# Performance work log

Hardware: AMD Instinct MI355X
Metric: run time of the kernel (lower is better)

Reference implementation:

```python
import jax, jax.numpy as jnp
import numpy as np

N = 100000   # nodes
E = 1600000  # edges
F = 128      # input features
H = 128      # hidden
L = 4        # num_layers (1 conv1 + 3 convs)
S = 10000    # subgraphs
G = 256      # graphs
C = 10       # classes
BN_EPS = 1e-5


def setup_inputs() -> dict:
    key = jax.random.key(0)
    ks = jax.random.split(key, 12)
    x = jax.random.normal(ks[0], (N, F), jnp.float32)
    edge_index = jax.random.randint(ks[1], (2, E), 0, N, jnp.int32)
    node_to_subgraph = jnp.sort(jax.random.randint(ks[2], (N,), 0, S, jnp.int32))
    subgraph_to_graph = jnp.sort(jax.random.randint(ks[3], (S,), 0, G, jnp.int32))
    sc = 1.0 / np.sqrt(H)
    # stacked per-layer GIN MLP params (torch Linear layout [out, in]); F == H so conv1 stacks too
    W1 = jax.random.uniform(ks[4], (L, H, F), jnp.float32, -sc, sc)
    b1 = jax.random.uniform(ks[5], (L, H), jnp.float32, -sc, sc)
    g1 = jnp.ones((L, H), jnp.float32)
    be1 = jnp.zeros((L, H), jnp.float32)
    W2 = jax.random.uniform(ks[6], (L, H, H), jnp.float32, -sc, sc)
    b2 = jax.random.uniform(ks[7], (L, H), jnp.float32, -sc, sc)
    g2 = jnp.ones((L, H), jnp.float32)
    be2 = jnp.zeros((L, H), jnp.float32)
    eps = jnp.zeros((L,), jnp.float32)  # train_eps=True, init 0
    sc1 = 1.0 / np.sqrt(L * H)
    lin1_W = jax.random.uniform(ks[8], (H, L * H), jnp.float32, -sc1, sc1)
    lin1_b = jax.random.uniform(ks[9], (H,), jnp.float32, -sc1, sc1)
    lin2_W = jax.random.uniform(ks[10], (C, H), jnp.float32, -sc, sc)
    lin2_b = jax.random.uniform(ks[11], (C,), jnp.float32, -sc, sc)
    return dict(x=x, edge_index=edge_index, node_to_subgraph=node_to_subgraph,
                subgraph_to_graph=subgraph_to_graph, W1=W1, b1=b1, g1=g1, be1=be1,
                W2=W2, b2=b2, g2=g2, be2=be2, eps=eps,
                lin1_W=lin1_W, lin1_b=lin1_b, lin2_W=lin2_W, lin2_b=lin2_b)


def _bn(h, g, b):
    mu = h.mean(axis=0)
    var = jnp.mean((h - mu) ** 2, axis=0)  # biased var (training-mode BN)
    return (h - mu) * jax.lax.rsqrt(var + BN_EPS) * g + b


def _seg_mean(f, seg, num_segments):
    s = jax.ops.segment_sum(f, seg, num_segments=num_segments)
    cnt = jax.ops.segment_sum(jnp.ones((f.shape[0], 1), f.dtype), seg, num_segments=num_segments)
    return s / jnp.maximum(cnt, 1.0)


def reference(x, edge_index, node_to_subgraph, subgraph_to_graph,
              W1, b1, g1, be1, W2, b2, g2, be2, eps,
              lin1_W, lin1_b, lin2_W, lin2_b):
    src, dst = edge_index[0], edge_index[1]

    def layer(xc, p):
        w1, bb1, gg1, bt1, w2, bb2, gg2, bt2, e = p
        agg = jax.ops.segment_sum(xc[src], dst, num_segments=N)  # neighbor sum
        h = (1.0 + e) * xc + agg
        h = jax.nn.relu(_bn(h @ w1.T + bb1, gg1, bt1))
        h = jax.nn.relu(_bn(h @ w2.T + bb2, gg2, bt2))
        return h, h

    _, ys = jax.lax.scan(layer, x, (W1, b1, g1, be1, W2, b2, g2, be2, eps))  # [L, N, H]
    feat = jnp.transpose(ys, (1, 0, 2)).reshape(N, L * H)  # torch.cat(xs, dim=1)
    sub = _seg_mean(feat, node_to_subgraph, S)   # [S, L*H]
    gph = _seg_mean(sub, subgraph_to_graph, G)   # [G, L*H]
    h = jax.nn.relu(gph @ lin1_W.T + lin1_b)
    out = h @ lin2_W.T + lin2_b                  # dropout inactive in eval
    return jax.nn.log_softmax(out, axis=-1)
```

## Files before the change

### kernel.cpp

```cpp
#include <hip/hip_runtime.h>

typedef unsigned int u32;
typedef unsigned short u16;

#define NN 100000
#define EE 1600000
#define SS 10000
#define GG 256
#define NSCAN ((NN + 1023) / 1024)
#define NCHUNK 16

#define O_W1   0
#define O_B1   65536
#define O_G1   66048
#define O_BE1  66560
#define O_W2   67072
#define O_B2   132608
#define O_G2   133120
#define O_BE2  133632
#define O_EPS  134144
#define O_L1W  134148
#define O_L1B  199684
#define O_L2W  199812
#define O_L2B  201092
#define NPAR   201102

typedef __bf16 bf16x8_t __attribute__((ext_vector_type(8)));
typedef float f32x4_t __attribute__((ext_vector_type(4)));
typedef u32 u32x4_t __attribute__((ext_vector_type(4)));

__device__ __forceinline__ float bf2f(u16 u) {
  union { u32 i; float f; } x; x.i = ((u32)u) << 16; return x.f;
}
__device__ __forceinline__ u16 f2bf(float f) {
  union { float f; u32 i; } x; x.f = f;
  u32 r = x.i + 0x7fffu + ((x.i >> 16) & 1u);
  return (u16)(r >> 16);
}
__device__ __forceinline__ int lbound(const int* __restrict__ a, int n, int key) {
  int lo = 0, hi = n;
  while (lo < hi) { int mid = (lo + hi) >> 1; if (a[mid] < key) lo = mid + 1; else hi = mid; }
  return lo;
}

__global__ void k_sniff(const u16* __restrict__ x, int* __restrict__ flag) {
  __shared__ int cnt;
  if (threadIdx.x == 0) cnt = 0;
  __syncthreads();
  int weird = 0;
  for (int i = threadIdx.x; i < 8192; i += 256) {
    u16 v = x[i];
    int e = (v >> 7) & 0xff;
    if (e >= 0xC0) weird++;
  }
  atomicAdd(&cnt, weird);
  __syncthreads();
  if (threadIdx.x == 0) *flag = (cnt > 64) ? 1 : 0;
}

__global__ __launch_bounds__(256) void k_cvt_params(
    const void* pW1, const void* pb1, const void* pg1, const void* pbe1,
    const void* pW2, const void* pb2, const void* pg2, const void* pbe2,
    const void* peps, const void* pl1w, const void* pl1b, const void* pl2w, const void* pl2b,
    const int* __restrict__ flagp, float* __restrict__ P) {
  int i = blockIdx.x * 256 + threadIdx.x;
  if (i >= NPAR) return;
  const void* src; int rel;
  if      (i < O_B1)  { src = pW1;  rel = i - O_W1; }
  else if (i < O_G1)  { src = pb1;  rel = i - O_B1; }
  else if (i < O_BE1) { src = pg1;  rel = i - O_G1; }
  else if (i < O_W2)  { src = pbe1; rel = i - O_BE1; }
  else if (i < O_B2)  { src = pW2;  rel = i - O_W2; }
  else if (i < O_G2)  { src = pb2;  rel = i - O_B2; }
  else if (i < O_BE2) { src = pg2;  rel = i - O_G2; }
  else if (i < O_EPS) { src = pbe2; rel = i - O_BE2; }
  else if (i < O_L1W) { src = peps; rel = i - O_EPS; }
  else if (i < O_L1B) { src = pl1w; rel = i - O_L1W; }
  else if (i < O_L2W) { src = pl1b; rel = i - O_L1B; }
  else if (i < O_L2B) { src = pl2w; rel = i - O_L2W; }
  else                { src = pl2b; rel = i - O_L2B; }
  float v = (*flagp) ? ((const float*)src)[rel] : bf2f(((const u16*)src)[rel]);
  P[i] = v;
}

__global__ __launch_bounds__(256) void k_cvtW(const float* __restrict__ P,
                                              u16* __restrict__ W1b, u16* __restrict__ W2b) {
  int i = blockIdx.x * 256 + threadIdx.x;
  if (i >= 131072) return;
  if (i < 65536) W1b[i] = f2bf(P[O_W1 + i]);
  else           W2b[i - 65536] = f2bf(P[O_W2 + i - 65536]);
}

__global__ __launch_bounds__(256) void k_prep(const void* __restrict__ x, const int* __restrict__ flagp,
                                              u16* __restrict__ Z0) {
  int i = blockIdx.x * 256 + threadIdx.x;
  if (i >= (NN * 128) / 8) return;
  if (*flagp) {
    const float4* xf = (const float4*)x;
    float4 a = xf[i * 2], b = xf[i * 2 + 1];
    u32x4_t o;
    o[0] = (u32)f2bf(a.x) | ((u32)f2bf(a.y) << 16);
    o[1] = (u32)f2bf(a.z) | ((u32)f2bf(a.w) << 16);
    o[2] = (u32)f2bf(b.x) | ((u32)f2bf(b.y) << 16);
    o[3] = (u32)f2bf(b.z) | ((u32)f2bf(b.w) << 16);
    *(u32x4_t*)(Z0 + i * 8) = o;
  } else {
    *(u32x4_t*)(Z0 + i * 8) = ((const u32x4_t*)x)[i];
  }
}

__global__ __launch_bounds__(256) void k_hist12(const int* __restrict__ src, const int* __restrict__ dst,
                                                int* __restrict__ cnt, int* __restrict__ cnt2) {
  int i = blockIdx.x * 256 + threadIdx.x;
  if (i >= EE) return;
  int d = dst[i], s = src[i];
  atomicAdd(&cnt[d], 1);
  atomicAdd(&cnt2[d * NCHUNK + (s >> 13)], 1);
}

__global__ __launch_bounds__(256) void k_scan1(const int* __restrict__ cnt, int* __restrict__ bsum) {
  __shared__ int sh[256];
  int base = blockIdx.x * 1024 + threadIdx.x * 4;
  int s = 0;
#pragma unroll
  for (int i = 0; i < 4; i++) { int idx = base + i; s += (idx < NN) ? cnt[idx] : 0; }
  sh[threadIdx.x] = s; __syncthreads();
  for (int o = 128; o > 0; o >>= 1) {
    if (threadIdx.x < o) sh[threadIdx.x] += sh[threadIdx.x + o];
    __syncthreads();
  }
  if (threadIdx.x == 0) bsum[blockIdx.x] = sh[0];
}

__global__ void k_scan2(int* __restrict__ bsum, int* __restrict__ off) {
  if (threadIdx.x == 0 && blockIdx.x == 0) {
    int run = 0;
    for (int i = 0; i < NSCAN; i++) { int v = bsum[i]; bsum[i] = run; run += v; }
    off[NN] = run;
  }
}

__global__ __launch_bounds__(256) void k_scan3(const int* __restrict__ cnt, const int* __restrict__ bsum,
                                               int* __restrict__ off) {
  __shared__ int sh[256];
  int base = blockIdx.x * 1024 + threadIdx.x * 4;
  int v[4]; int s = 0;
#pragma unroll
  for (int i = 0; i < 4; i++) { int idx = base + i; v[i] = (idx < NN) ? cnt[idx] : 0; s += v[i]; }
  sh[threadIdx.x] = s; __syncthreads();
  for (int o = 1; o < 256; o <<= 1) {
    int add = (threadIdx.x >= o) ? sh[threadIdx.x - o] : 0;
    __syncthreads();
    sh[threadIdx.x] += add;
    __syncthreads();
  }
  int run = sh[threadIdx.x] - s + bsum[blockIdx.x];
#pragma unroll
  for (int i = 0; i < 4; i++) { int idx = base + i; if (idx < NN) { off[idx] = run; run += v[i]; } }
}

__global__ __launch_bounds__(256) void k_start2(const int* __restrict__ off, const int* __restrict__ cnt2,
                                                int* __restrict__ start2) {
  int d = blockIdx.x * 256 + threadIdx.x;
  if (d >= NN) return;
  int base = off[d];
#pragma unroll
  for (int c = 0; c < NCHUNK; c++) {
    int s = cnt2[d * NCHUNK + c];
    start2[d * NCHUNK + c] = base;
    base += s;
  }
}

__global__ __launch_bounds__(256) void k_fill2(const int* __restrict__ src, const int* __restrict__ dst,
                                               int* __restrict__ start2, int* __restrict__ csr) {
  int i = blockIdx.x * 256 + threadIdx.x;
  if (i >= EE) return;
  int d = dst[i], s = src[i];
  int p = atomicAdd(&start2[d * NCHUNK + (s >> 13)], 1);
  csr[p] = s;
}

__global__ __launch_bounds__(256) void k_agg_gemm(
    const u16* __restrict__ Z, const int* __restrict__ off, const int* __restrict__ csr,
    const u16* __restrict__ Wb, const float* __restrict__ bias, const float* __restrict__ P,
    int layer, int mode, const float* __restrict__ st_prev, const float* __restrict__ gw,
    const float* __restrict__ bw, u16* __restrict__ H, float* __restrict__ st) {
  __shared__ __align__(16) u16 lds[4][16][136];
  __shared__ __align__(16) int shidx[4][512];
  int wave = threadIdx.x >> 6, lane = threadIdx.x & 63;
  int r0 = blockIdx.x * 64 + wave * 16;
  float ev = 1.0f + P[O_EPS + layer];
  const u32* zr = (const u32*)Z;

  int c0 = 2 * lane, c1 = 2 * lane + 1;
  float scl0 = 1.f, scl1 = 1.f, sh0 = 0.f, sh1 = 0.f, ncl = -3.0e38f;
  if (mode) {
    float mu0 = st_prev[c0] * (1.0f / NN);
    float v0 = fmaxf(st_prev[128 + c0] * (1.0f / NN) - mu0 * mu0, 0.f);
    scl0 = gw[c0] * rsqrtf(v0 + 1e-5f);
    sh0 = bw[c0] - mu0 * scl0;
    float mu1 = st_prev[c1] * (1.0f / NN);
    float v1 = fmaxf(st_prev[128 + c1] * (1.0f / NN) - mu1 * mu1, 0.f);
    scl1 = gw[c1] * rsqrtf(v1 + 1e-5f);
    sh1 = bw[c1] - mu1 * scl1;
    ncl = 0.f;
  }

  int offv = 0;
  if (lane <= 16) {
    int rr = r0 + lane; if (rr > NN) rr = NN; if (rr < 0) rr = 0;
    offv = off[rr];
  }
  int ebase = __shfl(offv, 0, 64);
  int eend  = __shfl(offv, 16, 64);
  int tn = eend - ebase;
  int nst = tn < 512 ? tn : 512;
  for (int i = lane; i < nst; i += 64) shidx[wave][i] = csr[ebase + i];

  for (int rr = 0; rr < 16; rr++) {
    int row = r0 + rr;
    float a0 = 0.f, a1 = 0.f;
    if (row < NN) {
      int s = __shfl(offv, rr, 64), e = __shfl(offv, rr + 1, 64);
      int n = e - s, b = s - ebase;
      u32 d = zr[row * 64 + lane];
      a0 = ev * fmaxf(fmaf(bf2f((u16)(d & 0xffffu)), scl0, sh0), ncl);
      a1 = ev * fmaxf(fmaf(bf2f((u16)(d >> 16)), scl1, sh1), ncl);
      const int* ip = (b + n <= 512) ? &shidx[wave][b] : &csr[s];
      int i = 0;
      for (; i + 7 < n; i += 8) {
        u32 dd[8];
#pragma unroll
        for (int j = 0; j < 8; j++) dd[j] = zr[ip[i + j] * 64 + lane];
#pragma unroll
        for (int j = 0; j < 8; j++) {
          a0 += fmaxf(fmaf(bf2f((u16)(dd[j] & 0xffffu)), scl0, sh0), ncl);
          a1 += fmaxf(fmaf(bf2f((u16)(dd[j] >> 16)), scl1, sh1), ncl);
        }
      }
      for (; i + 1 < n; i += 2) {
        u32 d0 = zr[ip[i] * 64 + lane];
        u32 d1 = zr[ip[i + 1] * 64 + lane];
        a0 += fmaxf(fmaf(bf2f((u16)(d0 & 0xffffu)), scl0, sh0), ncl) +
              fmaxf(fmaf(bf2f((u16)(d1 & 0xffffu)), scl1 * 0.f + scl0, sh0), ncl);
        a1 += fmaxf(fmaf(bf2f((u16)(d0 >> 16)), scl1, sh1), ncl) +
              fmaxf(fmaf(bf2f((u16)(d1 >> 16)), scl1, sh1), ncl);
      }
      if (i < n) {
        u32 d0 = zr[ip[i] * 64 + lane];
        a0 += fmaxf(fmaf(bf2f((u16)(d0 & 0xffffu)), scl0, sh0), ncl);
        a1 += fmaxf(fmaf(bf2f((u16)(d0 >> 16)), scl1, sh1), ncl);
      }
    }
    ((u32*)&lds[wave][rr][0])[lane] = (u32)f2bf(a0) | ((u32)f2bf(a1) << 16);
  }

  int nidx = lane & 15, q = lane >> 4;
  f32x4_t acc[8];
  f32x4_t z4 = {0.f, 0.f, 0.f, 0.f};
#pragma unroll
  for (int ot = 0; ot < 8; ot++) acc[ot] = z4;
#pragma unroll
  for (int ks = 0; ks < 4; ks++) {
    bf16x8_t af = __builtin_bit_cast(bf16x8_t, *(const u32x4_t*)&lds[wave][nidx][ks * 32 + q * 8]);
#pragma unroll
    for (int ot = 0; ot < 8; ot++) {
      bf16x8_t bfr = __builtin_bit_cast(bf16x8_t, *(const u32x4_t*)(Wb + (ot * 16 + nidx) * 128 + ks * 32 + q * 8));
      acc[ot] = __builtin_amdgcn_mfma_f32_16x16x32_bf16(af, bfr, acc[ot], 0, 0, 0);
    }
  }
  float* sstw = (float*)&shidx[wave][0];
#pragma unroll
  for (int ot = 0; ot < 8; ot++) {
    int col = ot * 16 + nidx;
    float bv = bias[col];
    float s = 0.f, sq = 0.f;
#pragma unroll
    for (int j = 0; j < 4; j++) {
      int row = r0 + q * 4 + j;
      if (row < NN) {
        float v = acc[ot][j] + bv;
        u16 h = f2bf(v);
        float vr = bf2f(h);
        H[row * 128 + col] = h;
        s += vr; sq += vr * vr;
      }
    }
    s  += __shfl_xor(s, 16, 64);  s  += __shfl_xor(s, 32, 64);
    sq += __shfl_xor(sq, 16, 64); sq += __shfl_xor(sq, 32, 64);
    if (q == 0) { sstw[col] = s; sstw[128 + col] = sq; }
  }
  __syncthreads();
  int t = threadIdx.x;
  float tot = ((float*)&shidx[0][0])[t] + ((float*)&shidx[1][0])[t] +
              ((float*)&shidx[2][0])[t] + ((float*)&shidx[3][0])[t];
  atomicAdd(&st[t], tot);
}

__global__ __launch_bounds__(256) void k_bn_gemm(
    const u16* __restrict__ Hin, const u16* __restrict__ Wb, const float* __restrict__ bias,
    const float* __restrict__ st_in, const float* __restrict__ gw, const float* __restrict__ bw,
    u16* __restrict__ Hout, float* __restrict__ st_out) {
  __shared__ float sc[256];
  __shared__ float sst[4][256];
  int t = threadIdx.x;
  if (t < 128) {
    float mu = st_in[t] * (1.0f / NN);
    float var = st_in[128 + t] * (1.0f / NN) - mu * mu;
    var = fmaxf(var, 0.f);
    float r = rsqrtf(var + 1e-5f);
    float scl = gw[t] * r;
    sc[t] = scl;
    sc[128 + t] = bw[t] - mu * scl;
  }
  __syncthreads();
  int wave = t >> 6, lane = t & 63;
  int r0 = blockIdx.x * 64 + wave * 16;
  int nidx = lane & 15, q = lane >> 4;
  int arow = r0 + nidx;
  u32x4_t zero4 = {0, 0, 0, 0};
  u32x4_t raw[4];
#pragma unroll
  for (int ks = 0; ks < 4; ks++)
    raw[ks] = (arow < NN) ? *(const u32x4_t*)(Hin + arow * 128 + ks * 32 + q * 8) : zero4;
  f32x4_t acc[8];
  f32x4_t z4 = {0.f, 0.f, 0.f, 0.f};
#pragma unroll
  for (int ot = 0; ot < 8; ot++) acc[ot] = z4;
#pragma unroll
  for (int ks = 0; ks < 4; ks++) {
    int k0 = ks * 32 + q * 8;
    u32x4_t ap;
#pragma unroll
    for (int w = 0; w < 4; w++) {
      int k = k0 + 2 * w;
      float v0 = fmaxf(bf2f((u16)(raw[ks][w] & 0xffffu)) * sc[k] + sc[128 + k], 0.f);
      float v1 = fmaxf(bf2f((u16)(raw[ks][w] >> 16)) * sc[k + 1] + sc[128 + k + 1], 0.f);
      ap[w] = (u32)f2bf(v0) | ((u32)f2bf(v1) << 16);
    }
    bf16x8_t af = __builtin_bit_cast(bf16x8_t, ap);
#pragma unroll
    for (int ot = 0; ot < 8; ot++) {
      bf16x8_t bfr = __builtin_bit_cast(bf16x8_t, *(const u32x4_t*)(Wb + (ot * 16 + nidx) * 128 + k0));
      acc[ot] = __builtin_amdgcn_mfma_f32_16x16x32_bf16(af, bfr, acc[ot], 0, 0, 0);
    }
  }
#pragma unroll
  for (int ot = 0; ot < 8; ot++) {
    int col = ot * 16 + nidx;
    float bv = bias[col];
    float s = 0.f, sq = 0.f;
#pragma unroll
    for (int j = 0; j < 4; j++) {
      int row = r0 + q * 4 + j;
      if (row < NN) {
        float v = acc[ot][j] + bv;
        u16 h = f2bf(v);
        float vr = bf2f(h);
        Hout[row * 128 + col] = h;
        s += vr; sq += vr * vr;
      }
    }
    s  += __shfl_xor(s, 16, 64);  s  += __shfl_xor(s, 32, 64);
    sq += __shfl_xor(sq, 16, 64); sq += __shfl_xor(sq, 32, 64);
    if (q == 0) { sst[wave][col] = s; sst[wave][128 + col] = sq; }
  }
  __syncthreads();
  float tot = sst[0][t] + sst[1][t] + sst[2][t] + sst[3][t];
  atomicAdd(&st_out[t], tot);
}

__global__ __launch_bounds__(256) void k_sub(
    const u16* __restrict__ Hin, const float* __restrict__ st_in, const float* __restrict__ gw,
    const float* __restrict__ bw, const int* __restrict__ n2s,
    float* __restrict__ sub, int layer) {
  __shared__ float sc[256];
  int t = threadIdx.x;
  if (t < 128) {
    float mu = st_in[t] * (1.0f / NN);
    float var = st_in[128 + t] * (1.0f / NN) - mu * mu;
    var = fmaxf(var, 0.f);
    float r = rsqrtf(var + 1e-5f);
    float scl = gw[t] * r;
    sc[t] = scl;
    sc[128 + t] = bw[t] - mu * scl;
  }
  __syncthreads();
  int s = (blockIdx.x * 256 + t) >> 6;
  int lane = t & 63;
  if (s >= SS) return;
  int r0 = lbound(n2s, NN, s), r1 = lbound(n2s, NN, s + 1);
  float scl0 = sc[2 * lane], scl1 = sc[2 * lane + 1];
  float sh0 = sc[128 + 2 * lane], sh1 = sc[128 + 2 * lane + 1];
  const u32* hr = (const u32*)Hin;
  float a0 = 0.f, a1 = 0.f;
  for (int r = r0; r < r1; r++) {
    u32 d = hr[r * 64 + lane];
    a0 += fmaxf(bf2f((u16)(d & 0xffffu)) * scl0 + sh0, 0.f);
    a1 += fmaxf(bf2f((u16)(d >> 16)) * scl1 + sh1, 0.f);
  }
  int c = r1 - r0;
  float inv = 1.0f / (float)(c > 0 ? c : 1);
  float2 v; v.x = a0 * inv; v.y = a1 * inv;
  *(float2*)(sub + (size_t)s * 512 + layer * 128 + lane * 2) = v;
}

__global__ __launch_bounds__(256) void k_graphpool(const float* __restrict__ sub, const int* __restrict__ s2g,
                                                   float* __restrict__ gph) {
  int g = (blockIdx.x * 256 + threadIdx.x) >> 6;
  int lane = threadIdx.x & 63;
  if (g >= GG) return;
  int r0 = lbound(s2g, SS, g), r1 = lbound(s2g, SS, g + 1);
  float a[8] = {0.f, 0.f, 0.f, 0.f, 0.f, 0.f, 0.f, 0.f};
  for (int s = r0; s < r1; s++) {
    const float* row = sub + (size_t)s * 512 + lane * 8;
#pragma unroll
    for (int j = 0; j < 8; j++) a[j] += row[j];
  }
  int c = r1 - r0;
  float inv = 1.0f / (float)(c > 0 ? c : 1);
  float* orow = gph + (size_t)g * 512 + lane * 8;
#pragma unroll
  for (int j = 0; j < 8; j++) orow[j] = a[j] * inv;
}

__global__ __launch_bounds__(128) void k_head(const float* __restrict__ gph, const float* __restrict__ P,
                                              const int* __restrict__ flagp, void* __restrict__ out) {
  __shared__ float gsh[512];
  __shared__ float hsh[128];
  __shared__ float lsh[12];
  int g = blockIdx.x, t = threadIdx.x;
  for (int i = t; i < 512; i += 128) gsh[i] = gph[(size_t)g * 512 + i];
  __syncthreads();
  float acc = P[O_L1B + t];
  const float4* wr = (const float4*)(P + O_L1W + t * 512);
  for (int kb = 0; kb < 128; kb++) {
    float4 w = wr[kb];
    int k = kb * 4;
    acc += gsh[k] * w.x + gsh[k + 1] * w.y + gsh[k + 2] * w.z + gsh[k + 3] * w.w;
  }
  hsh[t] = fmaxf(acc, 0.f);
  __syncthreads();
  if (t < 10) {
    float a = P[O_L2B + t];
    const float* w2r = P + O_L2W + t * 128;
    for (int k = 0; k < 128; k++) a += hsh[k] * w2r[k];
    lsh[t] = a;
  }
  __syncthreads();
  if (t == 0) {
    float m = -1e30f;
    for (int c = 0; c < 10; c++) m = fmaxf(m, lsh[c]);
    float se = 0.f;
    for (int c = 0; c < 10; c++) se += expf(lsh[c] - m);
    lsh[10] = m + logf(se);
  }
  __syncthreads();
  if (t < 10) {
    float v = lsh[t] - lsh[10];
    if (*flagp) ((float*)out)[g * 10 + t] = v;
    else        ((u16*)out)[g * 10 + t] = f2bf(v);
  }
}

extern "C" void kernel_launch(void* const* d_in, const int* in_sizes, int n_in,
                              void* d_out, int out_size, void* d_ws, size_t ws_size,
                              hipStream_t stream) {
  const void* x   = d_in[0];
  const int* ei   = (const int*)d_in[1];
  const int* n2s  = (const int*)d_in[2];
  const int* s2g  = (const int*)d_in[3];

  char* ws = (char*)d_ws;
  size_t o = 0;
  auto alloc = [&](size_t b) -> void* {
    void* p = ws + o;
    o += (b + 255) & ~(size_t)255;
    return p;
  };
  int* flag    = (int*)alloc(256);
  int* off     = (int*)alloc((NN + 1) * 4);
  int* cnt     = (int*)alloc(NN * 4);
  int* bsum    = (int*)alloc(NSCAN * 4);
  int* cnt2    = (int*)alloc((size_t)NN * NCHUNK * 4);
  int* start2  = (int*)alloc((size_t)NN * NCHUNK * 4);
  int* csr     = (int*)alloc((size_t)EE * 4);
  u16* Z0      = (u16*)alloc((size_t)NN * 128 * 2);
  u16* H1      = (u16*)alloc((size_t)NN * 128 * 2);
  u16* H2A     = (u16*)alloc((size_t)NN * 128 * 2);
  u16* H2B     = (u16*)alloc((size_t)NN * 128 * 2);
  float* sub   = (float*)alloc((size_t)SS * 512 * 4);
  float* gph   = (float*)alloc((size_t)GG * 512 * 4);
  float* stats = (float*)alloc(8 * 256 * 4);
  float* P     = (float*)alloc((size_t)NPAR * 4);
  u16* W1b     = (u16*)alloc(65536 * 2);
  u16* W2b     = (u16*)alloc(65536 * 2);

  const int* esrc = ei;
  const int* edst = ei + EE;

  hipMemsetAsync(cnt, 0, NN * 4, stream);
  hipMemsetAsync(cnt2, 0, (size_t)NN * NCHUNK * 4, stream);
  hipMemsetAsync(stats, 0, 8 * 256 * 4, stream);

  k_sniff<<<dim3(1), dim3(256), 0, stream>>>((const u16*)x, flag);
  k_cvt_params<<<dim3((NPAR + 255) / 256), dim3(256), 0, stream>>>(
      d_in[4], d_in[5], d_in[6], d_in[7], d_in[8], d_in[9], d_in[10], d_in[11],
      d_in[12], d_in[13], d_in[14], d_in[15], d_in[16], flag, P);
  k_cvtW<<<dim3(512), dim3(256), 0, stream>>>(P, W1b, W2b);
  k_prep<<<dim3((NN * 128 / 8 + 255) / 256), dim3(256), 0, stream>>>(x, flag, Z0);

  k_hist12<<<dim3((EE + 255) / 256), dim3(256), 0, stream>>>(esrc, edst, cnt, cnt2);
  k_scan1<<<dim3(NSCAN), dim3(256), 0, stream>>>(cnt, bsum);
  k_scan2<<<dim3(1), dim3(64), 0, stream>>>(bsum, off);
  k_scan3<<<dim3(NSCAN), dim3(256), 0, stream>>>(cnt, bsum, off);
  k_start2<<<dim3((NN + 255) / 256), dim3(256), 0, stream>>>(off, cnt2, start2);
  k_fill2<<<dim3((EE + 255) / 256), dim3(256), 0, stream>>>(esrc, edst, start2, csr);

  const u16* H2prev = Z0;
  for (int l = 0; l < 4; l++) {
    u16* H2cur = (l & 1) ? H2B : H2A;
    float* st1 = stats + (2 * l) * 256;
    float* st2 = stats + (2 * l + 1) * 256;
    const float* stp = (l > 0) ? (stats + (2 * l - 1) * 256) : P;
    k_agg_gemm<<<dim3((NN + 63) / 64), dim3(256), 0, stream>>>(
        H2prev, off, csr, W1b + l * 16384, P + O_B1 + l * 128, P, l,
        (l > 0) ? 1 : 0, stp, P + O_G2 + (l - 1 >= 0 ? l - 1 : 0) * 128,
        P + O_BE2 + (l - 1 >= 0 ? l - 1 : 0) * 128, H1, st1);
    k_bn_gemm<<<dim3((NN + 63) / 64), dim3(256), 0, stream>>>(
        H1, W2b + l * 16384, P + O_B2 + l * 128, st1, P + O_G1 + l * 128, P + O_BE1 + l * 128, H2cur, st2);
    k_sub<<<dim3((SS + 3) / 4), dim3(256), 0, stream>>>(
        H2cur, st2, P + O_G2 + l * 128, P + O_BE2 + l * 128, n2s, sub, l);
    H2prev = H2cur;
  }
  k_graphpool<<<dim3((GG + 3) / 4), dim3(256), 0, stream>>>(sub, s2g, gph);
  k_head<<<dim3(GG), dim3(128), 0, stream>>>(gph, P, flag, (void*)d_out);
}
```

Baseline: 1.318 ms.

## Gather neighbor rows as 16-byte vectors across four lane slots and simplify CSR build

The aggregation loop now has each lane load 8 bf16 features (16 bytes) per neighbor, with four 16-lane slots handling different neighbors in parallel, then reduces across slots with shuffles. The self term is folded in as neighbor index zero, and the mode flag becomes a template parameter so layer 0 skips the BN/ReLU math. The CSR build drops the per-source-chunk bucketing (cnt2/start2) in favor of a plain atomic fill, which removes a kernel and a large memset but loses the source-sorted neighbor order that may have helped gather locality.

```diff
diff --git a/kernel.cpp b/kernel.cpp
--- a/kernel.cpp
+++ b/kernel.cpp
@@ -8,7 +8,6 @@
 #define SS 10000
 #define GG 256
 #define NSCAN ((NN + 1023) / 1024)
-#define NCHUNK 16
 
 #define O_W1   0
 #define O_B1   65536
@@ -109,13 +108,9 @@
   }
 }
 
-__global__ __launch_bounds__(256) void k_hist12(const int* __restrict__ src, const int* __restrict__ dst,
-                                                int* __restrict__ cnt, int* __restrict__ cnt2) {
+__global__ __launch_bounds__(256) void k_hist(const int* __restrict__ dst, int* __restrict__ cnt) {
   int i = blockIdx.x * 256 + threadIdx.x;
-  if (i >= EE) return;
-  int d = dst[i], s = src[i];
-  atomicAdd(&cnt[d], 1);
-  atomicAdd(&cnt2[d * NCHUNK + (s >> 13)], 1);
+  if (i < EE) atomicAdd(&cnt[dst[i]], 1);
 }
 
 __global__ __launch_bounds__(256) void k_scan1(const int* __restrict__ cnt, int* __restrict__ bsum) {
@@ -159,52 +154,40 @@
   for (int i = 0; i < 4; i++) { int idx = base + i; if (idx < NN) { off[idx] = run; run += v[i]; } }
 }
 
-__global__ __launch_bounds__(256) void k_start2(const int* __restrict__ off, const int* __restrict__ cnt2,
-                                                int* __restrict__ start2) {
-  int d = blockIdx.x * 256 + threadIdx.x;
-  if (d >= NN) return;
-  int base = off[d];
-#pragma unroll
-  for (int c = 0; c < NCHUNK; c++) {
-    int s = cnt2[d * NCHUNK + c];
-    start2[d * NCHUNK + c] = base;
-    base += s;
-  }
-}
-
-__global__ __launch_bounds__(256) void k_fill2(const int* __restrict__ src, const int* __restrict__ dst,
-                                               int* __restrict__ start2, int* __restrict__ csr) {
+__global__ __launch_bounds__(256) void k_fill(const int* __restrict__ src, const int* __restrict__ dst,
+                                              const int* __restrict__ off, int* __restrict__ cur,
+                                              int* __restrict__ csr) {
   int i = blockIdx.x * 256 + threadIdx.x;
   if (i >= EE) return;
-  int d = dst[i], s = src[i];
-  int p = atomicAdd(&start2[d * NCHUNK + (s >> 13)], 1);
-  csr[p] = s;
-}
-
+  int d = dst[i];
+  int p = off[d] + atomicAdd(&cur[d], 1);
+  csr[p] = src[i];
+}
+
+template <int MODE>
 __global__ __launch_bounds__(256) void k_agg_gemm(
     const u16* __restrict__ Z, const int* __restrict__ off, const int* __restrict__ csr,
     const u16* __restrict__ Wb, const float* __restrict__ bias, const float* __restrict__ P,
-    int layer, int mode, const float* __restrict__ st_prev, const float* __restrict__ gw,
+    int layer, const float* __restrict__ st_prev, const float* __restrict__ gw,
     const float* __restrict__ bw, u16* __restrict__ H, float* __restrict__ st) {
   __shared__ __align__(16) u16 lds[4][16][136];
   __shared__ __align__(16) int shidx[4][512];
   int wave = threadIdx.x >> 6, lane = threadIdx.x & 63;
   int r0 = blockIdx.x * 64 + wave * 16;
   float ev = 1.0f + P[O_EPS + layer];
-  const u32* zr = (const u32*)Z;
-
-  int c0 = 2 * lane, c1 = 2 * lane + 1;
-  float scl0 = 1.f, scl1 = 1.f, sh0 = 0.f, sh1 = 0.f, ncl = -3.0e38f;
-  if (mode) {
-    float mu0 = st_prev[c0] * (1.0f / NN);
-    float v0 = fmaxf(st_prev[128 + c0] * (1.0f / NN) - mu0 * mu0, 0.f);
-    scl0 = gw[c0] * rsqrtf(v0 + 1e-5f);
-    sh0 = bw[c0] - mu0 * scl0;
-    float mu1 = st_prev[c1] * (1.0f / NN);
-    float v1 = fmaxf(st_prev[128 + c1] * (1.0f / NN) - mu1 * mu1, 0.f);
-    scl1 = gw[c1] * rsqrtf(v1 + 1e-5f);
-    sh1 = bw[c1] - mu1 * scl1;
-    ncl = 0.f;
+  int slot = lane >> 4;
+  int cb = (lane & 15) * 8;
+
+  float scl[8], shf[8];
+  if (MODE) {
+#pragma unroll
+    for (int k = 0; k < 8; k++) {
+      int c = cb + k;
+      float mu = st_prev[c] * (1.0f / NN);
+      float var = fmaxf(st_prev[128 + c] * (1.0f / NN) - mu * mu, 0.f);
+      float s = gw[c] * rsqrtf(var + 1e-5f);
+      scl[k] = s; shf[k] = bw[c] - mu * s;
+    }
   }
 
   int offv = 0;
@@ -220,40 +203,62 @@
 
   for (int rr = 0; rr < 16; rr++) {
     int row = r0 + rr;
-    float a0 = 0.f, a1 = 0.f;
+    float acc[8];
+#pragma unroll
+    for (int k = 0; k < 8; k++) acc[k] = 0.f;
     if (row < NN) {
       int s = __shfl(offv, rr, 64), e = __shfl(offv, rr + 1, 64);
       int n = e - s, b = s - ebase;
-      u32 d = zr[row * 64 + lane];
-      a0 = ev * fmaxf(fmaf(bf2f((u16)(d & 0xffffu)), scl0, sh0), ncl);
-      a1 = ev * fmaxf(fmaf(bf2f((u16)(d >> 16)), scl1, sh1), ncl);
-      const int* ip = (b + n <= 512) ? &shidx[wave][b] : &csr[s];
-      int i = 0;
-      for (; i + 7 < n; i += 8) {
-        u32 dd[8];
-#pragma unroll
-        for (int j = 0; j < 8; j++) dd[j] = zr[ip[i + j] * 64 + lane];
-#pragma unroll
-        for (int j = 0; j < 8; j++) {
-          a0 += fmaxf(fmaf(bf2f((u16)(dd[j] & 0xffffu)), scl0, sh0), ncl);
-          a1 += fmaxf(fmaf(bf2f((u16)(dd[j] >> 16)), scl1, sh1), ncl);
+      int m = n + 1;
+      auto nbr = [&](int j) -> int {
+        int t = b + j - 1;
+        return (t < 512) ? shidx[wave][t] : csr[ebase + t];
+      };
+      auto consume = [&](u32x4_t d, float c) {
+#pragma unroll
+        for (int k = 0; k < 4; k++) {
+          float v0 = bf2f((u16)(d[k] & 0xffffu));
+          float v1 = bf2f((u16)(d[k] >> 16));
+          if (MODE) {
+            v0 = fmaxf(fmaf(v0, scl[2 * k], shf[2 * k]), 0.f);
+            v1 = fmaxf(fmaf(v1, scl[2 * k + 1], shf[2 * k + 1]), 0.f);
+          }
+          acc[2 * k]     = fmaf(v0, c, acc[2 * k]);
+          acc[2 * k + 1] = fmaf(v1, c, acc[2 * k + 1]);
         }
+      };
+      int g = 0;
+      for (; g + 16 <= m; g += 16) {
+        int j0 = g + slot;
+        int i0 = (j0 == 0) ? row : nbr(j0);
+        int i1 = nbr(j0 + 4), i2 = nbr(j0 + 8), i3 = nbr(j0 + 12);
+        u32x4_t d0 = *(const u32x4_t*)(Z + (size_t)i0 * 128 + cb);
+        u32x4_t d1 = *(const u32x4_t*)(Z + (size_t)i1 * 128 + cb);
+        u32x4_t d2 = *(const u32x4_t*)(Z + (size_t)i2 * 128 + cb);
+        u32x4_t d3 = *(const u32x4_t*)(Z + (size_t)i3 * 128 + cb);
+        consume(d0, (j0 == 0) ? ev : 1.f);
+        consume(d1, 1.f); consume(d2, 1.f); consume(d3, 1.f);
       }
-      for (; i + 1 < n; i += 2) {
-        u32 d0 = zr[ip[i] * 64 + lane];
-        u32 d1 = zr[ip[i + 1] * 64 + lane];
-        a0 += fmaxf(fmaf(bf2f((u16)(d0 & 0xffffu)), scl0, sh0), ncl) +
-              fmaxf(fmaf(bf2f((u16)(d1 & 0xffffu)), scl1 * 0.f + scl0, sh0), ncl);
-        a1 += fmaxf(fmaf(bf2f((u16)(d0 >> 16)), scl1, sh1), ncl) +
-              fmaxf(fmaf(bf2f((u16)(d1 >> 16)), scl1, sh1), ncl);
+      for (; g < m; g += 4) {
+        int j = g + slot;
+        int idx = row; float c = 0.f;
+        if (j < m) { c = 1.f; if (j > 0) idx = nbr(j); else c = ev; }
+        u32x4_t d = *(const u32x4_t*)(Z + (size_t)idx * 128 + cb);
+        consume(d, c);
       }
-      if (i < n) {
-        u32 d0 = zr[ip[i] * 64 + lane];
-        a0 += fmaxf(fmaf(bf2f((u16)(d0 & 0xffffu)), scl0, sh0), ncl);
-        a1 += fmaxf(fmaf(bf2f((u16)(d0 >> 16)), scl1, sh1), ncl);
+#pragma unroll
+      for (int k = 0; k < 8; k++) {
+        acc[k] += __shfl_xor(acc[k], 16, 64);
+        acc[k] += __shfl_xor(acc[k], 32, 64);
       }
     }
-    ((u32*)&lds[wave][rr][0])[lane] = (u32)f2bf(a0) | ((u32)f2bf(a1) << 16);
+    if (lane < 16) {
+      u32x4_t o;
+#pragma unroll
+      for (int k = 0; k < 4; k++)
+        o[k] = (u32)f2bf(acc[2 * k]) | ((u32)f2bf(acc[2 * k + 1]) << 16);
+      *(u32x4_t*)&lds[wave][rr][cb] = o;
+    }
   }
 
   int nidx = lane & 15, q = lane >> 4;
@@ -483,8 +488,6 @@
   int* off     = (int*)alloc((NN + 1) * 4);
   int* cnt     = (int*)alloc(NN * 4);
   int* bsum    = (int*)alloc(NSCAN * 4);
-  int* cnt2    = (int*)alloc((size_t)NN * NCHUNK * 4);
-  int* start2  = (int*)alloc((size_t)NN * NCHUNK * 4);
   int* csr     = (int*)alloc((size_t)EE * 4);
   u16* Z0      = (u16*)alloc((size_t)NN * 128 * 2);
   u16* H1      = (u16*)alloc((size_t)NN * 128 * 2);
@@ -501,7 +504,6 @@
   const int* edst = ei + EE;
 
   hipMemsetAsync(cnt, 0, NN * 4, stream);
-  hipMemsetAsync(cnt2, 0, (size_t)NN * NCHUNK * 4, stream);
   hipMemsetAsync(stats, 0, 8 * 256 * 4, stream);
 
   k_sniff<<<dim3(1), dim3(256), 0, stream>>>((const u16*)x, flag);
@@ -511,23 +513,26 @@
   k_cvtW<<<dim3(512), dim3(256), 0, stream>>>(P, W1b, W2b);
   k_prep<<<dim3((NN * 128 / 8 + 255) / 256), dim3(256), 0, stream>>>(x, flag, Z0);
 
-  k_hist12<<<dim3((EE + 255) / 256), dim3(256), 0, stream>>>(esrc, edst, cnt, cnt2);
+  k_hist<<<dim3((EE + 255) / 256), dim3(256), 0, stream>>>(edst, cnt);
   k_scan1<<<dim3(NSCAN), dim3(256), 0, stream>>>(cnt, bsum);
   k_scan2<<<dim3(1), dim3(64), 0, stream>>>(bsum, off);
   k_scan3<<<dim3(NSCAN), dim3(256), 0, stream>>>(cnt, bsum, off);
-  k_start2<<<dim3((NN + 255) / 256), dim3(256), 0, stream>>>(off, cnt2, start2);
-  k_fill2<<<dim3((EE + 255) / 256), dim3(256), 0, stream>>>(esrc, edst, start2, csr);
+  hipMemsetAsync(cnt, 0, NN * 4, stream);
+  k_fill<<<dim3((EE + 255) / 256), dim3(256), 0, stream>>>(esrc, edst, off, cnt, csr);
 
   const u16* H2prev = Z0;
   for (int l = 0; l < 4; l++) {
     u16* H2cur = (l & 1) ? H2B : H2A;
     float* st1 = stats + (2 * l) * 256;
     float* st2 = stats + (2 * l + 1) * 256;
-    const float* stp = (l > 0) ? (stats + (2 * l - 1) * 256) : P;
-    k_agg_gemm<<<dim3((NN + 63) / 64), dim3(256), 0, stream>>>(
-        H2prev, off, csr, W1b + l * 16384, P + O_B1 + l * 128, P, l,
-        (l > 0) ? 1 : 0, stp, P + O_G2 + (l - 1 >= 0 ? l - 1 : 0) * 128,
-        P + O_BE2 + (l - 1 >= 0 ? l - 1 : 0) * 128, H1, st1);
+    if (l == 0) {
+      k_agg_gemm<0><<<dim3((NN + 63) / 64), dim3(256), 0, stream>>>(
+          H2prev, off, csr, W1b, P + O_B1, P, 0, P, P, P, H1, st1);
+    } else {
+      k_agg_gemm<1><<<dim3((NN + 63) / 64), dim3(256), 0, stream>>>(
+          H2prev, off, csr, W1b + l * 16384, P + O_B1 + l * 128, P, l,
+          stats + (2 * l - 1) * 256, P + O_G2 + (l - 1) * 128, P + O_BE2 + (l - 1) * 128, H1, st1);
+    }
     k_bn_gemm<<<dim3((NN + 63) / 64), dim3(256), 0, stream>>>(
         H1, W2b + l * 16384, P + O_B2 + l * 128, st1, P + O_G1 + l * 128, P + O_BE1 + l * 128, H2cur, st2);
     k_sub<<<dim3((SS + 3) / 4), dim3(256), 0, stream>>>(
```

Result: faster. 1.274 ms (-3.4%).

## Gather neighbors chunk-major across a wave's 16 rows for cache locality

Applied to the files above, without the earlier changes.

The aggregation loop now walks source-index chunks (8192-node ranges) in the outer loop and the wave's 16 destination rows in the inner loop, using per-row chunk boundaries staged in shared memory. The goal is to keep the gathered source rows within a narrow address window at a time and improve L2 hit rate. The degree count is now derived from the chunk histogram, which drops one atomic histogram. The kernel is also templated on the BN/ReLU mode. The gather loop loses its 8-way unrolled batching of independent loads, so memory-level parallelism per lane drops and 32 float accumulators add register pressure.

```diff
diff --git a/kernel.cpp b/kernel.cpp
--- a/kernel.cpp
+++ b/kernel.cpp
@@ -8,7 +8,7 @@
 #define SS 10000
 #define GG 256
 #define NSCAN ((NN + 1023) / 1024)
-#define NCHUNK 16
+#define NCH 13
 
 #define O_W1   0
 #define O_B1   65536
@@ -109,21 +109,26 @@
   }
 }
 
-__global__ __launch_bounds__(256) void k_hist12(const int* __restrict__ src, const int* __restrict__ dst,
-                                                int* __restrict__ cnt, int* __restrict__ cnt2) {
+__global__ __launch_bounds__(256) void k_hist2(const int* __restrict__ src, const int* __restrict__ dst,
+                                               int* __restrict__ cnt2) {
   int i = blockIdx.x * 256 + threadIdx.x;
   if (i >= EE) return;
-  int d = dst[i], s = src[i];
-  atomicAdd(&cnt[d], 1);
-  atomicAdd(&cnt2[d * NCHUNK + (s >> 13)], 1);
-}
-
-__global__ __launch_bounds__(256) void k_scan1(const int* __restrict__ cnt, int* __restrict__ bsum) {
+  atomicAdd(&cnt2[dst[i] * 16 + (src[i] >> 13)], 1);
+}
+
+__device__ __forceinline__ int rowdeg(const int* __restrict__ cnt2, int row) {
+  const int4* p = (const int4*)(cnt2 + row * 16);
+  int4 q0 = p[0], q1 = p[1], q2 = p[2];
+  return q0.x + q0.y + q0.z + q0.w + q1.x + q1.y + q1.z + q1.w +
+         q2.x + q2.y + q2.z + q2.w + cnt2[row * 16 + 12];
+}
+
+__global__ __launch_bounds__(256) void k_scan1(const int* __restrict__ cnt2, int* __restrict__ bsum) {
   __shared__ int sh[256];
   int base = blockIdx.x * 1024 + threadIdx.x * 4;
   int s = 0;
 #pragma unroll
-  for (int i = 0; i < 4; i++) { int idx = base + i; s += (idx < NN) ? cnt[idx] : 0; }
+  for (int i = 0; i < 4; i++) { int idx = base + i; if (idx < NN) s += rowdeg(cnt2, idx); }
   sh[threadIdx.x] = s; __syncthreads();
   for (int o = 128; o > 0; o >>= 1) {
     if (threadIdx.x < o) sh[threadIdx.x] += sh[threadIdx.x + o];
@@ -140,13 +145,17 @@
   }
 }
 
-__global__ __launch_bounds__(256) void k_scan3(const int* __restrict__ cnt, const int* __restrict__ bsum,
+__global__ __launch_bounds__(256) void k_scan3(const int* __restrict__ cnt2, const int* __restrict__ bsum,
                                                int* __restrict__ off) {
   __shared__ int sh[256];
   int base = blockIdx.x * 1024 + threadIdx.x * 4;
   int v[4]; int s = 0;
 #pragma unroll
-  for (int i = 0; i < 4; i++) { int idx = base + i; v[i] = (idx < NN) ? cnt[idx] : 0; s += v[i]; }
+  for (int i = 0; i < 4; i++) {
+    int idx = base + i;
+    v[i] = (idx < NN) ? rowdeg(cnt2, idx) : 0;
+    s += v[i];
+  }
   sh[threadIdx.x] = s; __syncthreads();
   for (int o = 1; o < 256; o <<= 1) {
     int add = (threadIdx.x >= o) ? sh[threadIdx.x - o] : 0;
@@ -160,51 +169,54 @@
 }
 
 __global__ __launch_bounds__(256) void k_start2(const int* __restrict__ off, const int* __restrict__ cnt2,
-                                                int* __restrict__ start2) {
+                                                int* __restrict__ start2, int* __restrict__ cur2) {
   int d = blockIdx.x * 256 + threadIdx.x;
   if (d >= NN) return;
   int base = off[d];
 #pragma unroll
-  for (int c = 0; c < NCHUNK; c++) {
-    int s = cnt2[d * NCHUNK + c];
-    start2[d * NCHUNK + c] = base;
+  for (int c = 0; c < NCH; c++) {
+    int s = cnt2[d * 16 + c];
+    start2[d * 16 + c] = base;
+    cur2[d * 16 + c] = base;
     base += s;
   }
 }
 
 __global__ __launch_bounds__(256) void k_fill2(const int* __restrict__ src, const int* __restrict__ dst,
-                                               int* __restrict__ start2, int* __restrict__ csr) {
+                                               int* __restrict__ cur2, int* __restrict__ csr) {
   int i = blockIdx.x * 256 + threadIdx.x;
   if (i >= EE) return;
   int d = dst[i], s = src[i];
-  int p = atomicAdd(&start2[d * NCHUNK + (s >> 13)], 1);
+  int p = atomicAdd(&cur2[d * 16 + (s >> 13)], 1);
   csr[p] = s;
 }
 
+template <int MODE>
 __global__ __launch_bounds__(256) void k_agg_gemm(
-    const u16* __restrict__ Z, const int* __restrict__ off, const int* __restrict__ csr,
-    const u16* __restrict__ Wb, const float* __restrict__ bias, const float* __restrict__ P,
-    int layer, int mode, const float* __restrict__ st_prev, const float* __restrict__ gw,
-    const float* __restrict__ bw, u16* __restrict__ H, float* __restrict__ st) {
+    const u16* __restrict__ Z, const int* __restrict__ off, const int* __restrict__ start2,
+    const int* __restrict__ csr, const u16* __restrict__ Wb, const float* __restrict__ bias,
+    const float* __restrict__ P, int layer, const float* __restrict__ st_prev,
+    const float* __restrict__ gw, const float* __restrict__ bw,
+    u16* __restrict__ H, float* __restrict__ st) {
   __shared__ __align__(16) u16 lds[4][16][136];
   __shared__ __align__(16) int shidx[4][512];
+  __shared__ int sbound[4][16][NCH + 1];
   int wave = threadIdx.x >> 6, lane = threadIdx.x & 63;
   int r0 = blockIdx.x * 64 + wave * 16;
   float ev = 1.0f + P[O_EPS + layer];
   const u32* zr = (const u32*)Z;
 
-  int c0 = 2 * lane, c1 = 2 * lane + 1;
-  float scl0 = 1.f, scl1 = 1.f, sh0 = 0.f, sh1 = 0.f, ncl = -3.0e38f;
-  if (mode) {
-    float mu0 = st_prev[c0] * (1.0f / NN);
-    float v0 = fmaxf(st_prev[128 + c0] * (1.0f / NN) - mu0 * mu0, 0.f);
-    scl0 = gw[c0] * rsqrtf(v0 + 1e-5f);
-    sh0 = bw[c0] - mu0 * scl0;
-    float mu1 = st_prev[c1] * (1.0f / NN);
-    float v1 = fmaxf(st_prev[128 + c1] * (1.0f / NN) - mu1 * mu1, 0.f);
-    scl1 = gw[c1] * rsqrtf(v1 + 1e-5f);
-    sh1 = bw[c1] - mu1 * scl1;
-    ncl = 0.f;
+  int cc0 = 2 * lane, cc1 = 2 * lane + 1;
+  float scl0 = 1.f, scl1 = 1.f, sh0 = 0.f, sh1 = 0.f;
+  if (MODE) {
+    float mu0 = st_prev[cc0] * (1.0f / NN);
+    float v0 = fmaxf(st_prev[128 + cc0] * (1.0f / NN) - mu0 * mu0, 0.f);
+    scl0 = gw[cc0] * rsqrtf(v0 + 1e-5f);
+    sh0 = bw[cc0] - mu0 * scl0;
+    float mu1 = st_prev[cc1] * (1.0f / NN);
+    float v1 = fmaxf(st_prev[128 + cc1] * (1.0f / NN) - mu1 * mu1, 0.f);
+    scl1 = gw[cc1] * rsqrtf(v1 + 1e-5f);
+    sh1 = bw[cc1] - mu1 * scl1;
   }
 
   int offv = 0;
@@ -218,43 +230,52 @@
   int nst = tn < 512 ? tn : 512;
   for (int i = lane; i < nst; i += 64) shidx[wave][i] = csr[ebase + i];
 
+  for (int i = lane; i < 16 * (NCH + 1); i += 64) {
+    int rr = i / (NCH + 1), c = i - rr * (NCH + 1);
+    int row = r0 + rr;
+    int v = ebase;
+    if (row < NN) v = (c < NCH) ? start2[row * 16 + c] : off[row + 1];
+    sbound[wave][rr][c] = v - ebase;
+  }
+
+  float a0[16], a1[16];
+#pragma unroll
   for (int rr = 0; rr < 16; rr++) {
     int row = r0 + rr;
-    float a0 = 0.f, a1 = 0.f;
+    float x0 = 0.f, x1 = 0.f;
     if (row < NN) {
-      int s = __shfl(offv, rr, 64), e = __shfl(offv, rr + 1, 64);
-      int n = e - s, b = s - ebase;
       u32 d = zr[row * 64 + lane];
-      a0 = ev * fmaxf(fmaf(bf2f((u16)(d & 0xffffu)), scl0, sh0), ncl);
-      a1 = ev * fmaxf(fmaf(bf2f((u16)(d >> 16)), scl1, sh1), ncl);
-      const int* ip = (b + n <= 512) ? &shidx[wave][b] : &csr[s];
-      int i = 0;
-      for (; i + 7 < n; i += 8) {
-        u32 dd[8];
-#pragma unroll
-        for (int j = 0; j < 8; j++) dd[j] = zr[ip[i + j] * 64 + lane];
-#pragma unroll
-        for (int j = 0; j < 8; j++) {
-          a0 += fmaxf(fmaf(bf2f((u16)(dd[j] & 0xffffu)), scl0, sh0), ncl);
-          a1 += fmaxf(fmaf(bf2f((u16)(dd[j] >> 16)), scl1, sh1), ncl);
+      x0 = bf2f((u16)(d & 0xffffu));
+      x1 = bf2f((u16)(d >> 16));
+      if (MODE) {
+        x0 = fmaxf(fmaf(x0, scl0, sh0), 0.f);
+        x1 = fmaxf(fmaf(x1, scl1, sh1), 0.f);
+      }
+    }
+    a0[rr] = ev * x0; a1[rr] = ev * x1;
+  }
+
+  for (int c = 0; c < NCH; c++) {
+#pragma unroll
+    for (int rr = 0; rr < 16; rr++) {
+      int s = sbound[wave][rr][c], e = sbound[wave][rr][c + 1];
+      for (int i = s; i < e; i++) {
+        int idx = (i < 512) ? shidx[wave][i] : csr[ebase + i];
+        u32 d = zr[idx * 64 + lane];
+        float v0 = bf2f((u16)(d & 0xffffu));
+        float v1 = bf2f((u16)(d >> 16));
+        if (MODE) {
+          v0 = fmaxf(fmaf(v0, scl0, sh0), 0.f);
+          v1 = fmaxf(fmaf(v1, scl1, sh1), 0.f);
         }
+        a0[rr] += v0; a1[rr] += v1;
       }
-      for (; i + 1 < n; i += 2) {
-        u32 d0 = zr[ip[i] * 64 + lane];
-        u32 d1 = zr[ip[i + 1] * 64 + lane];
-        a0 += fmaxf(fmaf(bf2f((u16)(d0 & 0xffffu)), scl0, sh0), ncl) +
-              fmaxf(fmaf(bf2f((u16)(d1 & 0xffffu)), scl1 * 0.f + scl0, sh0), ncl);
-        a1 += fmaxf(fmaf(bf2f((u16)(d0 >> 16)), scl1, sh1), ncl) +
-              fmaxf(fmaf(bf2f((u16)(d1 >> 16)), scl1, sh1), ncl);
-      }
-      if (i < n) {
-        u32 d0 = zr[ip[i] * 64 + lane];
-        a0 += fmaxf(fmaf(bf2f((u16)(d0 & 0xffffu)), scl0, sh0), ncl);
-        a1 += fmaxf(fmaf(bf2f((u16)(d0 >> 16)), scl1, sh1), ncl);
-      }
-    }
-    ((u32*)&lds[wave][rr][0])[lane] = (u32)f2bf(a0) | ((u32)f2bf(a1) << 16);
-  }
+    }
+  }
+
+#pragma unroll
+  for (int rr = 0; rr < 16; rr++)
+    ((u32*)&lds[wave][rr][0])[lane] = (u32)f2bf(a0[rr]) | ((u32)f2bf(a1[rr]) << 16);
 
   int nidx = lane & 15, q = lane >> 4;
   f32x4_t acc[8];
@@ -481,10 +502,10 @@
   };
   int* flag    = (int*)alloc(256);
   int* off     = (int*)alloc((NN + 1) * 4);
-  int* cnt     = (int*)alloc(NN * 4);
   int* bsum    = (int*)alloc(NSCAN * 4);
-  int* cnt2    = (int*)alloc((size_t)NN * NCHUNK * 4);
-  int* start2  = (int*)alloc((size_t)NN * NCHUNK * 4);
+  int* cnt2    = (int*)alloc((size_t)NN * 16 * 4);
+  int* start2  = (int*)alloc((size_t)NN * 16 * 4);
+  int* cur2    = (int*)alloc((size_t)NN * 16 * 4);
   int* csr     = (int*)alloc((size_t)EE * 4);
   u16* Z0      = (u16*)alloc((size_t)NN * 128 * 2);
   u16* H1      = (u16*)alloc((size_t)NN * 128 * 2);
@@ -500,8 +521,7 @@
   const int* esrc = ei;
   const int* edst = ei + EE;
 
-  hipMemsetAsync(cnt, 0, NN * 4, stream);
-  hipMemsetAsync(cnt2, 0, (size_t)NN * NCHUNK * 4, stream);
+  hipMemsetAsync(cnt2, 0, (size_t)NN * 16 * 4, stream);
   hipMemsetAsync(stats, 0, 8 * 256 * 4, stream);
 
   k_sniff<<<dim3(1), dim3(256), 0, stream>>>((const u16*)x, flag);
@@ -511,23 +531,26 @@
   k_cvtW<<<dim3(512), dim3(256), 0, stream>>>(P, W1b, W2b);
   k_prep<<<dim3((NN * 128 / 8 + 255) / 256), dim3(256), 0, stream>>>(x, flag, Z0);
 
-  k_hist12<<<dim3((EE + 255) / 256), dim3(256), 0, stream>>>(esrc, edst, cnt, cnt2);
-  k_scan1<<<dim3(NSCAN), dim3(256), 0, stream>>>(cnt, bsum);
+  k_hist2<<<dim3((EE + 255) / 256), dim3(256), 0, stream>>>(esrc, edst, cnt2);
+  k_scan1<<<dim3(NSCAN), dim3(256), 0, stream>>>(cnt2, bsum);
   k_scan2<<<dim3(1), dim3(64), 0, stream>>>(bsum, off);
-  k_scan3<<<dim3(NSCAN), dim3(256), 0, stream>>>(cnt, bsum, off);
-  k_start2<<<dim3((NN + 255) / 256), dim3(256), 0, stream>>>(off, cnt2, start2);
-  k_fill2<<<dim3((EE + 255) / 256), dim3(256), 0, stream>>>(esrc, edst, start2, csr);
+  k_scan3<<<dim3(NSCAN), dim3(256), 0, stream>>>(cnt2, bsum, off);
+  k_start2<<<dim3((NN + 255) / 256), dim3(256), 0, stream>>>(off, cnt2, start2, cur2);
+  k_fill2<<<dim3((EE + 255) / 256), dim3(256), 0, stream>>>(esrc, edst, cur2, csr);
 
   const u16* H2prev = Z0;
   for (int l = 0; l < 4; l++) {
     u16* H2cur = (l & 1) ? H2B : H2A;
     float* st1 = stats + (2 * l) * 256;
     float* st2 = stats + (2 * l + 1) * 256;
-    const float* stp = (l > 0) ? (stats + (2 * l - 1) * 256) : P;
-    k_agg_gemm<<<dim3((NN + 63) / 64), dim3(256), 0, stream>>>(
-        H2prev, off, csr, W1b + l * 16384, P + O_B1 + l * 128, P, l,
-        (l > 0) ? 1 : 0, stp, P + O_G2 + (l - 1 >= 0 ? l - 1 : 0) * 128,
-        P + O_BE2 + (l - 1 >= 0 ? l - 1 : 0) * 128, H1, st1);
+    if (l == 0) {
+      k_agg_gemm<0><<<dim3((NN + 63) / 64), dim3(256), 0, stream>>>(
+          H2prev, off, start2, csr, W1b, P + O_B1, P, 0, P, P, P, H1, st1);
+    } else {
+      k_agg_gemm<1><<<dim3((NN + 63) / 64), dim3(256), 0, stream>>>(
+          H2prev, off, start2, csr, W1b + l * 16384, P + O_B1 + l * 128, P, l,
+          stats + (2 * l - 1) * 256, P + O_G2 + (l - 1) * 128, P + O_BE2 + (l - 1) * 128, H1, st1);
+    }
     k_bn_gemm<<<dim3((NN + 63) / 64), dim3(256), 0, stream>>>(
         H1, W2b + l * 16384, P + O_B2 + l * 128, st1, P + O_G1 + l * 128, P + O_BE1 + l * 128, H2cur, st2);
     k_sub<<<dim3((SS + 3) / 4), dim3(256), 0, stream>>>(
```

After: 1.796 ms. 36.2% more time.
